# Optimization experiments

Hardware: AMD Instinct MI355X
Metric: run time of the kernel (lower is better)

## Reference

```python
import jax, jax.numpy as jnp
import numpy as np

T, B, H, E, V, L = 256, 32, 1024, 1024, 32000, 2


def lstm_stack(x, h0, c0, Wih, Whh, bih, bhh):
    # x: [T,B,E]; Wih/Whh: [L,4H,H]; bih/bhh: [L,4H]; h0/c0: [L,B,H]
    for l in range(Wih.shape[0]):
        Wi, Wh, bi, bh = Wih[l], Whh[l], bih[l], bhh[l]

        def step(carry, xt, Wi=Wi, Wh=Wh, bi=bi, bh=bh):
            h, c = carry
            g = xt @ Wi.T + h @ Wh.T + bi + bh  # [B,4H]
            i_, f_, g_, o_ = jnp.split(g, 4, axis=-1)  # PyTorch gate order i,f,g,o
            c = jax.nn.sigmoid(f_) * c + jax.nn.sigmoid(i_) * jnp.tanh(g_)
            h = jax.nn.sigmoid(o_) * jnp.tanh(c)
            return (h, c), h

        (_, _), x = jax.lax.scan(step, (h0[l], c0[l]), x)
    return x  # [T,B,H]


def setup_inputs() -> dict:
    key = jax.random.key(0)
    ks = jax.random.split(key, 20)
    u = lambda k, s: jax.random.uniform(k, s, jnp.float32, -0.1, 0.1)
    n = lambda k, s: 0.02 * jax.random.normal(k, s, jnp.float32)
    return {
        'data_left': jax.random.randint(ks[0], (T, B), 0, V),
        'data_right': jax.random.randint(ks[1], (T, B), 0, V),
        'h0_left': jnp.zeros((L, B, H), jnp.float32),
        'c0_left': jnp.zeros((L, B, H), jnp.float32),
        'h0_right': jnp.zeros((L, B, H), jnp.float32),
        'c0_right': jnp.zeros((L, B, H), jnp.float32),
        'emb': u(ks[2], (V, E)),
        'Wih_l': n(ks[3], (L, 4 * H, H)), 'Whh_l': n(ks[4], (L, 4 * H, H)),
        'bih_l': n(ks[5], (L, 4 * H)), 'bhh_l': n(ks[6], (L, 4 * H)),
        'Wih_r': n(ks[7], (L, 4 * H, H)), 'Whh_r': n(ks[8], (L, 4 * H, H)),
        'bih_r': n(ks[9], (L, 4 * H)), 'bhh_r': n(ks[10], (L, 4 * H)),
        'attn_w': n(ks[11], (1, 3 * H)), 'attn_b': n(ks[12], (1,)),
        'trans_w': n(ks[13], (H, 3 * H)), 'trans_b': n(ks[14], (H,)),
        'dec_w': u(ks[15], (V, H)), 'dec_b': jnp.zeros((V,), jnp.float32),
    }


def reference(data_left, data_right, h0_left, c0_left, h0_right, c0_right,
              emb, Wih_l, Whh_l, bih_l, bhh_l, Wih_r, Whh_r, bih_r, bhh_r,
              attn_w, attn_b, trans_w, trans_b, dec_w, dec_b):
    # Encode (dropout=0 -> identity). Right branch runs on the flipped sequence.
    xL = emb[data_left]                    # [T,B,E]
    xR = emb[data_right[::-1]]             # [T,B,E]
    outL = lstm_stack(xL, h0_left, c0_left, Wih_l, Whh_l, bih_l, bhh_l)   # [T,B,H]
    outR = lstm_stack(xR, h0_right, c0_right, Wih_r, Whh_r, bih_r, bhh_r)[::-1]

    # attn Linear(3H,1) splits into per-chunk projections: [left_i, right_i, ctx_k]
    w1, w2, w3 = jnp.split(attn_w[0], 3)   # each [H]
    a = outL @ w1 + outR @ w2 + attn_b[0]  # [T,B] query-dependent part
    sL = outL @ w3                          # [T,B]
    sR = outR @ w3                          # [T,B]

    # context for query i has fixed length T+1: k<=i -> outL[k], k>i -> outR[k-1]
    kk = jnp.arange(T + 1)
    ii = jnp.arange(T)
    maskL = kk[None, :] <= ii[:, None]      # [T,T+1]
    sL_pad = jnp.concatenate([sL, jnp.zeros((1, B), sL.dtype)], 0)   # [T+1,B]
    sR_sh = jnp.concatenate([jnp.zeros((1, B), sR.dtype), sR], 0)    # sR[k-1]
    ctx_s = jnp.where(maskL[:, :, None], sL_pad[None], sR_sh[None])  # [T,T+1,B]
    scores = jnp.tanh(a[:, None, :] + ctx_s)                          # [T,T+1,B]
    p = jax.nn.softmax(scores, axis=1)

    pL = p * maskL[:, :, None]
    pR = p * (~maskL)[:, :, None]
    # context_vector[i] = sum_k p[i,k] * ctx[i,k]
    cv = (jnp.einsum('ikb,kbh->ibh', pL[:, :T], outL)
          + jnp.einsum('ikb,kbh->ibh', pR[:, 1:], outR))              # [T,B,H]

    h3 = jnp.concatenate([outL, outR, cv], axis=-1)                   # [T,B,3H]
    pred = jnp.tanh(h3 @ trans_w.T + trans_b)                         # [T,B,H]
    decoded = pred @ dec_w.T + dec_b                                  # [T,B,V]
    return decoded
```

## Files before the change

### kernel.cpp

```cpp
#include <hip/hip_runtime.h>
#include <hip/hip_bf16.h>


using bf16 = __hip_bfloat16;
typedef __attribute__((ext_vector_type(8))) __bf16 bf16x8;
typedef __attribute__((ext_vector_type(4))) float f32x4;
typedef __attribute__((ext_vector_type(4))) short short4v;

#define T_ 256
#define B_ 32
#define H_ 1024
#define V_ 32000

__device__ __forceinline__ float b2f(bf16 x) { return __bfloat162float(x); }
__device__ __forceinline__ bf16 f2b(float x) { return __float2bfloat16(x); }
__device__ __forceinline__ float us2f(unsigned short u) {
  union { unsigned u; float f; } w; w.u = ((unsigned)u) << 16; return w.f;
}
__device__ __forceinline__ void st4(bf16* dst, float4 f) {
  union { bf16 h[4]; short4v s; } u;
  u.h[0] = f2b(f.x); u.h[1] = f2b(f.y); u.h[2] = f2b(f.z); u.h[3] = f2b(f.w);
  *reinterpret_cast<short4v*>(dst) = u.s;
}
__device__ __forceinline__ bf16x8 cvt8(float4 a, float4 b) {
  union { bf16 h[8]; bf16x8 v; } u;
  u.h[0] = f2b(a.x); u.h[1] = f2b(a.y); u.h[2] = f2b(a.z); u.h[3] = f2b(a.w);
  u.h[4] = f2b(b.x); u.h[5] = f2b(b.y); u.h[6] = f2b(b.z); u.h[7] = f2b(b.w);
  return u.v;
}

__global__ __launch_bounds__(256)
void cvt_f32_bf16(const float* __restrict__ src, bf16* __restrict__ dst, long n)
{
  long i = ((long)blockIdx.x * 256 + threadIdx.x) * 8;
  if (i >= n) return;
  float4 a = *reinterpret_cast<const float4*>(src + i);
  float4 b = *reinterpret_cast<const float4*>(src + i + 4);
  st4(dst + i, a); st4(dst + i + 4, b);
}

__global__ __launch_bounds__(128)
void embed_gather(const int* __restrict__ dl, const int* __restrict__ dr,
                  const float* __restrict__ emb,
                  bf16* __restrict__ xL, bf16* __restrict__ xR)
{
  int wg = blockIdx.x;
  int d  = wg >> 13;
  int r  = wg & 8191;
  int t  = r >> 5, b = r & 31;
  int tok = d ? dr[(T_ - 1 - t) * B_ + b] : dl[r];
  const float* src = emb + (long)tok * H_;
  bf16* dst = (d ? xR : xL) + (long)r * H_;
  int e = threadIdx.x * 8;
  float4 a = *reinterpret_cast<const float4*>(src + e);
  float4 c = *reinterpret_cast<const float4*>(src + e + 4);
  st4(dst + e, a); st4(dst + e + 4, c);
}

#define LSTRIDE 40

template<int ACT, int HASBIAS, int OUTF32>
__global__ __launch_bounds__(256)
void gemm_bt(const bf16* __restrict__ A, const float* __restrict__ Bwf,
             const float* __restrict__ bias, void* __restrict__ Cv,
             int M, int N, int K)
{
  __shared__ __align__(16) bf16 As[128 * LSTRIDE];
  __shared__ __align__(16) bf16 Bs[128 * LSTRIDE];
  const int tid  = threadIdx.x;
  const int lane = tid & 63;
  const int wave = tid >> 6;
  const int wm = wave >> 1, wn = wave & 1;
  const long bm = blockIdx.x, bn = blockIdx.y;

  const bf16*  Ag = A + bm * 128 * (long)K;
  const float* Bg = Bwf + bn * 128 * (long)K;

  f32x4 acc[4][4] = {};

  const int nk = K >> 5;
  for (int kt = 0; kt < nk; ++kt) {
    const int k0 = kt * 32;
    __syncthreads();
    #pragma unroll
    for (int j = 0; j < 2; ++j) {
      int chunk = j * 256 + tid;
      int row = chunk >> 2, c4 = chunk & 3;
      *reinterpret_cast<bf16x8*>(&As[row * LSTRIDE + c4 * 8]) =
          *reinterpret_cast<const bf16x8*>(&Ag[(long)row * K + k0 + c4 * 8]);
    }
    #pragma unroll
    for (int j = 0; j < 4; ++j) {
      int chunk = j * 256 + tid;
      int row = chunk >> 3, c4f = chunk & 7;
      float4 f = *reinterpret_cast<const float4*>(&Bg[(long)row * K + k0 + c4f * 4]);
      st4(&Bs[row * LSTRIDE + c4f * 4], f);
    }
    __syncthreads();
    bf16x8 af[4], bfr[4];
    #pragma unroll
    for (int m = 0; m < 4; ++m)
      af[m] = *reinterpret_cast<const bf16x8*>(
          &As[(wm * 64 + m * 16 + (lane & 15)) * LSTRIDE + (lane >> 4) * 8]);
    #pragma unroll
    for (int n = 0; n < 4; ++n)
      bfr[n] = *reinterpret_cast<const bf16x8*>(
          &Bs[(wn * 64 + n * 16 + (lane & 15)) * LSTRIDE + (lane >> 4) * 8]);
    #pragma unroll
    for (int m = 0; m < 4; ++m)
      #pragma unroll
      for (int n = 0; n < 4; ++n)
        acc[m][n] = __builtin_amdgcn_mfma_f32_16x16x32_bf16(af[m], bfr[n], acc[m][n], 0, 0, 0);
  }

  #pragma unroll
  for (int m = 0; m < 4; ++m) {
    int row = (int)bm * 128 + wm * 64 + m * 16 + ((lane >> 4) << 2);
    #pragma unroll
    for (int n = 0; n < 4; ++n) {
      int col = (int)bn * 128 + wn * 64 + n * 16 + (lane & 15);
      float bv = HASBIAS ? bias[col] : 0.f;
      #pragma unroll
      for (int j = 0; j < 4; ++j) {
        float v = acc[m][n][j] + bv;
        if (ACT) v = tanhf(v);
        long off = (long)(row + j) * N + col;
        if (OUTF32) reinterpret_cast<float*>(Cv)[off] = v;
        else        reinterpret_cast<bf16*>(Cv)[off] = f2b(v);
      }
    }
  }
}

__global__ __launch_bounds__(256, 1)
void lstm_layer(const bf16* __restrict__ WhhL, const bf16* __restrict__ WhhR,
                const bf16* __restrict__ giL,  const bf16* __restrict__ giR,
                const float* __restrict__ bihL, const float* __restrict__ bhhL,
                const float* __restrict__ bihR, const float* __restrict__ bhhR,
                const float* __restrict__ h0L, const float* __restrict__ h0R,
                const float* __restrict__ c0L, const float* __restrict__ c0R,
                bf16* __restrict__ houtL, bf16* __restrict__ houtR,
                int revR, unsigned* __restrict__ bar)
{
  const int d    = blockIdx.y;
  const int u0   = blockIdx.x * 16;
  const int tid  = threadIdx.x;
  const int lane = tid & 63;
  const int wq   = tid >> 6;
  const long BH  = (long)B_ * H_;

  const bf16*  Whh = d ? WhhR : WhhL;
  const bf16*  gi0 = d ? giR  : giL;
  const float* bi  = d ? bihR : bihL;
  const float* bh  = d ? bhhR : bhhL;
  const float* h0  = d ? h0R  : h0L;
  const float* c0  = d ? c0R  : c0L;
  bf16* hout       = d ? houtR : houtL;
  const int rev    = d ? revR : 0;
  unsigned* cnt    = bar + d;

  (void)__hip_atomic_load(cnt, __ATOMIC_ACQUIRE, __HIP_MEMORY_SCOPE_AGENT);

  const int klo = (lane >> 4) * 8;

  bf16x8 w_reg[4][8];
  #pragma unroll
  for (int g = 0; g < 4; ++g) {
    const bf16* p = Whh + ((long)g * H_ + u0 + (lane & 15)) * H_ + wq * 256 + klo;
    #pragma unroll
    for (int q = 0; q < 8; ++q)
      w_reg[g][q] = *reinterpret_cast<const bf16x8*>(p + q * 32);
  }

  const int b  = tid >> 3;
  const int u  = (tid & 7) * 2;
  const int ug = u0 + u;

  float bsum[4][2];
  #pragma unroll
  for (int g = 0; g < 4; ++g) {
    bsum[g][0] = bi[g * H_ + ug]     + bh[g * H_ + ug];
    bsum[g][1] = bi[g * H_ + ug + 1] + bh[g * H_ + ug + 1];
  }
  float cc0 = c0[(long)b * H_ + ug];
  float cc1 = c0[(long)b * H_ + ug + 1];

  __shared__ float gbuf[4][4][32][16];

  for (int s = 0; s < T_; ++s) {
    unsigned giv[4];
    {
      const bf16* gis = gi0 + (long)s * (B_ * 4 * H_) + (long)b * (4 * H_);
      #pragma unroll
      for (int g = 0; g < 4; ++g)
        giv[g] = *reinterpret_cast<const unsigned*>(&gis[g * H_ + ug]);
    }

    f32x4 acc[4][2];
    #pragma unroll
    for (int g = 0; g < 4; ++g) {
      acc[g][0] = f32x4{0.f, 0.f, 0.f, 0.f};
      acc[g][1] = f32x4{0.f, 0.f, 0.f, 0.f};
    }

    if (s == 0) {
      const float* ap0 = h0 + (long)(lane & 15) * H_ + wq * 256 + klo;
      const float* ap1 = ap0 + 16L * H_;
      #pragma unroll
      for (int q = 0; q < 8; ++q) {
        bf16x8 a0 = cvt8(*reinterpret_cast<const float4*>(ap0 + q * 32),
                         *reinterpret_cast<const float4*>(ap0 + q * 32 + 4));
        bf16x8 a1 = cvt8(*reinterpret_cast<const float4*>(ap1 + q * 32),
                         *reinterpret_cast<const float4*>(ap1 + q * 32 + 4));
        #pragma unroll
        for (int g = 0; g < 4; ++g) {
          acc[g][0] = __builtin_amdgcn_mfma_f32_16x16x32_bf16(a0, w_reg[g][q], acc[g][0], 0, 0, 0);
          acc[g][1] = __builtin_amdgcn_mfma_f32_16x16x32_bf16(a1, w_reg[g][q], acc[g][1], 0, 0, 0);
        }
      }
    } else {
      const bf16* hp  = hout + (long)(rev ? (T_ - s) : (s - 1)) * BH;
      const bf16* ap0 = hp + (long)(lane & 15) * H_ + wq * 256 + klo;
      const bf16* ap1 = ap0 + 16L * H_;
      #pragma unroll
      for (int q = 0; q < 8; ++q) {
        bf16x8 a0 = *reinterpret_cast<const bf16x8*>(ap0 + q * 32);
        bf16x8 a1 = *reinterpret_cast<const bf16x8*>(ap1 + q * 32);
        #pragma unroll
        for (int g = 0; g < 4; ++g) {
          acc[g][0] = __builtin_amdgcn_mfma_f32_16x16x32_bf16(a0, w_reg[g][q], acc[g][0], 0, 0, 0);
          acc[g][1] = __builtin_amdgcn_mfma_f32_16x16x32_bf16(a1, w_reg[g][q], acc[g][1], 0, 0, 0);
        }
      }
    }

    {
      int cr = (lane >> 4) << 2, ccu = lane & 15;
      #pragma unroll
      for (int g = 0; g < 4; ++g)
        #pragma unroll
        for (int j = 0; j < 4; ++j) {
          gbuf[wq][g][cr + j][ccu]      = acc[g][0][j];
          gbuf[wq][g][16 + cr + j][ccu] = acc[g][1][j];
        }
    }
    __syncthreads();

    {
      float g4[4][2];
      #pragma unroll
      for (int g = 0; g < 4; ++g) {
        float p0 = gbuf[0][g][b][u]     + gbuf[1][g][b][u];
        float p1 = gbuf[2][g][b][u]     + gbuf[3][g][b][u];
        float q0 = gbuf[0][g][b][u + 1] + gbuf[1][g][b][u + 1];
        float q1 = gbuf[2][g][b][u + 1] + gbuf[3][g][b][u + 1];
        g4[g][0] = (p0 + p1) + us2f((unsigned short)(giv[g] & 0xffffu)) + bsum[g][0];
        g4[g][1] = (q0 + q1) + us2f((unsigned short)(giv[g] >> 16))     + bsum[g][1];
      }
      float si0 = 1.f / (1.f + expf(-g4[0][0])), si1 = 1.f / (1.f + expf(-g4[0][1]));
      float sf0 = 1.f / (1.f + expf(-g4[1][0])), sf1 = 1.f / (1.f + expf(-g4[1][1]));
      float tg0 = tanhf(g4[2][0]),               tg1 = tanhf(g4[2][1]);
      float so0 = 1.f / (1.f + expf(-g4[3][0])), so1 = 1.f / (1.f + expf(-g4[3][1]));
      cc0 = sf0 * cc0 + si0 * tg0;
      cc1 = sf1 * cc1 + si1 * tg1;
      float hn0 = so0 * tanhf(cc0);
      float hn1 = so1 * tanhf(cc1);
      union { bf16 h[2]; unsigned w; } up;
      up.h[0] = f2b(hn0); up.h[1] = f2b(hn1);
      long wIdx = rev ? (long)(T_ - 1 - s) : (long)s;
      __hip_atomic_store(
          reinterpret_cast<unsigned*>(&hout[wIdx * BH + (long)b * H_ + ug]),
          up.w, __ATOMIC_RELAXED, __HIP_MEMORY_SCOPE_AGENT);
    }

    if (s + 1 < T_) {
      __syncthreads();
      if (tid == 0) {
        __hip_atomic_fetch_add(cnt, 1u, __ATOMIC_RELAXED, __HIP_MEMORY_SCOPE_AGENT);
        unsigned tgt = 64u * (unsigned)(s + 1);
        while (__hip_atomic_load(cnt, __ATOMIC_RELAXED, __HIP_MEMORY_SCOPE_AGENT) < tgt)
          __builtin_amdgcn_s_sleep(2);
      }
      __syncthreads();
    }
  }
}

__global__ __launch_bounds__(256)
void attn_scores(const bf16* __restrict__ outL, const bf16* __restrict__ outR,
                 const float* __restrict__ attn_w, const float* __restrict__ attn_b,
                 float* __restrict__ a, float* __restrict__ sL, float* __restrict__ sR)
{
  int r = blockIdx.x;
  int tid = threadIdx.x;
  const bf16* oL = outL + (long)r * H_;
  const bf16* oR = outR + (long)r * H_;
  int e = tid * 4;
  float pa = 0.f, pl = 0.f, pr = 0.f;
  #pragma unroll
  for (int j = 0; j < 4; ++j) {
    float l_ = b2f(oL[e + j]), r_ = b2f(oR[e + j]);
    float w1 = attn_w[e + j];
    float w2 = attn_w[H_ + e + j];
    float w3 = attn_w[2 * H_ + e + j];
    pa += w1 * l_ + w2 * r_;
    pl += w3 * l_;
    pr += w3 * r_;
  }
  #pragma unroll
  for (int off = 32; off > 0; off >>= 1) {
    pa += __shfl_down(pa, off);
    pl += __shfl_down(pl, off);
    pr += __shfl_down(pr, off);
  }
  __shared__ float red[3][4];
  int wave = tid >> 6, lane = tid & 63;
  if (lane == 0) { red[0][wave] = pa; red[1][wave] = pl; red[2][wave] = pr; }
  __syncthreads();
  if (tid == 0) {
    a[r]  = red[0][0] + red[0][1] + red[0][2] + red[0][3] + attn_b[0];
    sL[r] = red[1][0] + red[1][1] + red[1][2] + red[1][3];
    sR[r] = red[2][0] + red[2][1] + red[2][2] + red[2][3];
  }
}

__global__ __launch_bounds__(64)
void attn_softmax(const float* __restrict__ a, const float* __restrict__ sL,
                  const float* __restrict__ sR, float* __restrict__ p)
{
  int i = blockIdx.x, b = blockIdx.y;
  int lane = threadIdx.x;
  float av = a[i * B_ + b];
  float sc[5];
  float mx = -1e30f;
  #pragma unroll
  for (int q = 0; q < 5; ++q) {
    int k = lane + q * 64;
    float v = -1e30f;
    if (k < 257) {
      float ctx = (k <= i) ? sL[k * B_ + b] : sR[(k - 1) * B_ + b];
      v = tanhf(av + ctx);
    }
    sc[q] = v;
    mx = fmaxf(mx, v);
  }
  #pragma unroll
  for (int off = 32; off > 0; off >>= 1) mx = fmaxf(mx, __shfl_xor(mx, off));
  float sum = 0.f;
  #pragma unroll
  for (int q = 0; q < 5; ++q) {
    int k = lane + q * 64;
    float e = (k < 257) ? __expf(sc[q] - mx) : 0.f;
    sc[q] = e; sum += e;
  }
  #pragma unroll
  for (int off = 32; off > 0; off >>= 1) sum += __shfl_xor(sum, off);
  float inv = 1.f / sum;
  long base = ((long)b * T_ + i) * 257;
  #pragma unroll
  for (int q = 0; q < 5; ++q) {
    int k = lane + q * 64;
    if (k < 257) p[base + k] = sc[q] * inv;
  }
}

__global__ __launch_bounds__(256)
void h3_copy(const bf16* __restrict__ outL, const bf16* __restrict__ outR,
             bf16* __restrict__ h3)
{
  long gid = (long)blockIdx.x * 256 + threadIdx.x;
  long e = gid * 8;
  if (e >= (long)T_ * B_ * H_) return;
  long r = e >> 10; int h = (int)(e & 1023);
  *reinterpret_cast<bf16x8*>(&h3[r * 3 * H_ + h]) =
      *reinterpret_cast<const bf16x8*>(&outL[e]);
  *reinterpret_cast<bf16x8*>(&h3[r * 3 * H_ + H_ + h]) =
      *reinterpret_cast<const bf16x8*>(&outR[e]);
}

__global__ __launch_bounds__(256)
void attn_cv(const float* __restrict__ p, const bf16* __restrict__ outL,
             const bf16* __restrict__ outR, bf16* __restrict__ h3)
{
  int b = blockIdx.y;
  int i0 = blockIdx.x * 16;
  int tid = threadIdx.x;
  __shared__ float ps[16][257];
  for (int idx = tid; idx < 16 * 257; idx += 256) {
    int ii = idx / 257, k = idx % 257;
    ps[ii][k] = p[((long)b * T_ + i0 + ii) * 257 + k];
  }
  __syncthreads();
  float acc[16][4] = {};
  int h0 = tid * 4;
  for (int k = 0; k < 257; ++k) {
    float vL[4] = {0.f, 0.f, 0.f, 0.f}, vR[4] = {0.f, 0.f, 0.f, 0.f};
    if (k < 256) {
      short4v v = *reinterpret_cast<const short4v*>(&outL[((long)k * B_ + b) * H_ + h0]);
      vL[0] = us2f((unsigned short)v[0]); vL[1] = us2f((unsigned short)v[1]);
      vL[2] = us2f((unsigned short)v[2]); vL[3] = us2f((unsigned short)v[3]);
    }
    if (k >= 1) {
      short4v v = *reinterpret_cast<const short4v*>(&outR[((long)(k - 1) * B_ + b) * H_ + h0]);
      vR[0] = us2f((unsigned short)v[0]); vR[1] = us2f((unsigned short)v[1]);
      vR[2] = us2f((unsigned short)v[2]); vR[3] = us2f((unsigned short)v[3]);
    }
    #pragma unroll
    for (int ii = 0; ii < 16; ++ii) {
      float pv = ps[ii][k];
      bool useL = (i0 + ii) >= k;
      #pragma unroll
      for (int j = 0; j < 4; ++j)
        acc[ii][j] += pv * (useL ? vL[j] : vR[j]);
    }
  }
  #pragma unroll
  for (int ii = 0; ii < 16; ++ii)
    #pragma unroll
    for (int j = 0; j < 4; ++j)
      h3[((long)(i0 + ii) * B_ + b) * 3 * H_ + 2 * H_ + h0 + j] = f2b(acc[ii][j]);
}

extern "C" void kernel_launch(void* const* d_in, const int* in_sizes, int n_in,
                              void* d_out, int out_size, void* d_ws, size_t ws_size,
                              hipStream_t stream)
{
  (void)in_sizes; (void)n_in; (void)out_size; (void)ws_size;
  const int*   data_left  = (const int*)  d_in[0];
  const int*   data_right = (const int*)  d_in[1];
  const float* h0_left    = (const float*)d_in[2];
  const float* c0_left    = (const float*)d_in[3];
  const float* h0_right   = (const float*)d_in[4];
  const float* c0_right   = (const float*)d_in[5];
  const float* emb        = (const float*)d_in[6];
  const float* Wih_l      = (const float*)d_in[7];
  const float* Whh_l      = (const float*)d_in[8];
  const float* bih_l      = (const float*)d_in[9];
  const float* bhh_l      = (const float*)d_in[10];
  const float* Wih_r      = (const float*)d_in[11];
  const float* Whh_r      = (const float*)d_in[12];
  const float* bih_r      = (const float*)d_in[13];
  const float* bhh_r      = (const float*)d_in[14];
  const float* attn_w     = (const float*)d_in[15];
  const float* attn_b     = (const float*)d_in[16];
  const float* trans_w    = (const float*)d_in[17];
  const float* trans_b    = (const float*)d_in[18];
  const float* dec_w      = (const float*)d_in[19];
  const float* dec_b      = (const float*)d_in[20];

  char* ws = (char*)d_ws;
  bf16*     XL   = (bf16*)    (ws + 0L);
  bf16*     XR   = (bf16*)    (ws + 16777216L);
  bf16*     GI_L = (bf16*)    (ws + 33554432L);
  bf16*     GI_R = (bf16*)    (ws + 100663296L);
  bf16*     H0L  = (bf16*)    (ws + 167772160L);
  bf16*     H0R  = (bf16*)    (ws + 184549376L);
  unsigned* BAR  = (unsigned*)(ws + 201326592L);
  bf16*     WHHB = (bf16*)    (ws + 201588736L);
  bf16*  O1L  = XL;
  bf16*  O1R  = XR;
  bf16*  H3   = GI_L;
  float* P_   = (float*)(ws + 100663296L);
  float* A_   = (float*)(ws + 109084672L);
  float* SL_  = (float*)(ws + 109117440L);
  float* SR_  = (float*)(ws + 109150208L);
  bf16*  PRED = (bf16*) (ws + 109182976L);

  const long BH  = (long)B_ * H_;
  const long WL  = 4L * H_ * H_;
  bf16* WHHB_l = WHHB;
  bf16* WHHB_r = WHHB + 2 * WL;

  cvt_f32_bf16<<<4096, 256, 0, stream>>>(Whh_l, WHHB_l, 2 * WL);
  cvt_f32_bf16<<<4096, 256, 0, stream>>>(Whh_r, WHHB_r, 2 * WL);

  embed_gather<<<16384, 128, 0, stream>>>(data_left, data_right, emb, XL, XR);

  gemm_bt<0,0,0><<<dim3(64, 32), 256, 0, stream>>>(XL, Wih_l, nullptr, GI_L, 8192, 4096, 1024);
  gemm_bt<0,0,0><<<dim3(64, 32), 256, 0, stream>>>(XR, Wih_r, nullptr, GI_R, 8192, 4096, 1024);

  hipMemsetAsync(BAR, 0, 64, stream);
  lstm_layer<<<dim3(64, 2), 256, 0, stream>>>(
      WHHB_l, WHHB_r, GI_L, GI_R,
      bih_l, bhh_l, bih_r, bhh_r,
      h0_left, h0_right, c0_left, c0_right,
      H0L, H0R, 0, BAR);

  gemm_bt<0,0,0><<<dim3(64, 32), 256, 0, stream>>>(H0L, Wih_l + WL, nullptr, GI_L, 8192, 4096, 1024);
  gemm_bt<0,0,0><<<dim3(64, 32), 256, 0, stream>>>(H0R, Wih_r + WL, nullptr, GI_R, 8192, 4096, 1024);

  hipMemsetAsync(BAR, 0, 64, stream);
  lstm_layer<<<dim3(64, 2), 256, 0, stream>>>(
      WHHB_l + WL, WHHB_r + WL, GI_L, GI_R,
      bih_l + 4 * H_, bhh_l + 4 * H_, bih_r + 4 * H_, bhh_r + 4 * H_,
      h0_left + BH, h0_right + BH, c0_left + BH, c0_right + BH,
      O1L, O1R, 1, BAR);

  attn_scores<<<8192, 256, 0, stream>>>(O1L, O1R, attn_w, attn_b, A_, SL_, SR_);
  attn_softmax<<<dim3(256, 32), 64, 0, stream>>>(A_, SL_, SR_, P_);
  h3_copy<<<4096, 256, 0, stream>>>(O1L, O1R, H3);
  attn_cv<<<dim3(16, 32), 256, 0, stream>>>(P_, O1L, O1R, H3);

  gemm_bt<1,1,0><<<dim3(64, 8),   256, 0, stream>>>(H3,   trans_w, trans_b, PRED, 8192, 1024, 3072);
  gemm_bt<0,1,1><<<dim3(64, 250), 256, 0, stream>>>(PRED, dec_w,   dec_b,   d_out, 8192, 32000, 1024);
}
```

Measured before the change: 4.784 ms.

## Fuse both LSTM layers into one wavefront-pipelined persistent kernel

Replaces the two sequential lstm_layer launches and the layer-1 input-projection GEMMs with a single persistent kernel of 384 blocks, split into three roles: layer-0 recurrence, a per-timestep layer-1 input projection that writes into a 4-slot ring buffer, and layer-1 recurrence. The roles synchronise through global atomic counters and per-block flags. Layer 1 can then run one step behind layer 0 instead of waiting for the whole of layer 0, which hides most of one full recurrent pass. In exchange, the layer-1 input projection becomes a small per-step MFMA job rather than a large efficient GEMM. Correctness depends on all 384 blocks being co-resident (two per CU under the launch bounds), and the extra spin-wait synchronisation adds per-step latency.

```diff
diff --git a/kernel.cpp b/kernel.cpp
--- a/kernel.cpp
+++ b/kernel.cpp
@@ -27,6 +27,10 @@
   u.h[0] = f2b(a.x); u.h[1] = f2b(a.y); u.h[2] = f2b(a.z); u.h[3] = f2b(a.w);
   u.h[4] = f2b(b.x); u.h[5] = f2b(b.y); u.h[6] = f2b(b.z); u.h[7] = f2b(b.w);
   return u.v;
+}
+__device__ __forceinline__ void poll_ge(unsigned* p, unsigned tgt) {
+  while (__hip_atomic_load(p, __ATOMIC_RELAXED, __HIP_MEMORY_SCOPE_AGENT) < tgt)
+    __builtin_amdgcn_s_sleep(2);
 }
 
 __global__ __launch_bounds__(256)
@@ -132,36 +136,149 @@
   }
 }
 
-__global__ __launch_bounds__(256, 1)
-void lstm_layer(const bf16* __restrict__ WhhL, const bf16* __restrict__ WhhR,
-                const bf16* __restrict__ giL,  const bf16* __restrict__ giR,
-                const float* __restrict__ bihL, const float* __restrict__ bhhL,
-                const float* __restrict__ bihR, const float* __restrict__ bhhR,
-                const float* __restrict__ h0L, const float* __restrict__ h0R,
-                const float* __restrict__ c0L, const float* __restrict__ c0R,
-                bf16* __restrict__ houtL, bf16* __restrict__ houtR,
-                int revR, unsigned* __restrict__ bar)
-{
-  const int d    = blockIdx.y;
-  const int u0   = blockIdx.x * 16;
+__device__ __forceinline__ void mfma_h_bf16(const bf16* hp, int lane, int wq, int klo,
+                                            const bf16x8 w[4][8], f32x4 acc[4][2])
+{
+  const bf16* ap0 = hp + (long)(lane & 15) * H_ + wq * 256 + klo;
+  const bf16* ap1 = ap0 + 16L * H_;
+  #pragma unroll
+  for (int q = 0; q < 8; ++q) {
+    bf16x8 a0 = *reinterpret_cast<const bf16x8*>(ap0 + q * 32);
+    bf16x8 a1 = *reinterpret_cast<const bf16x8*>(ap1 + q * 32);
+    #pragma unroll
+    for (int g = 0; g < 4; ++g) {
+      acc[g][0] = __builtin_amdgcn_mfma_f32_16x16x32_bf16(a0, w[g][q], acc[g][0], 0, 0, 0);
+      acc[g][1] = __builtin_amdgcn_mfma_f32_16x16x32_bf16(a1, w[g][q], acc[g][1], 0, 0, 0);
+    }
+  }
+}
+__device__ __forceinline__ void mfma_h_f32(const float* hp, int lane, int wq, int klo,
+                                           const bf16x8 w[4][8], f32x4 acc[4][2])
+{
+  const float* ap0 = hp + (long)(lane & 15) * H_ + wq * 256 + klo;
+  const float* ap1 = ap0 + 16L * H_;
+  #pragma unroll
+  for (int q = 0; q < 8; ++q) {
+    bf16x8 a0 = cvt8(*reinterpret_cast<const float4*>(ap0 + q * 32),
+                     *reinterpret_cast<const float4*>(ap0 + q * 32 + 4));
+    bf16x8 a1 = cvt8(*reinterpret_cast<const float4*>(ap1 + q * 32),
+                     *reinterpret_cast<const float4*>(ap1 + q * 32 + 4));
+    #pragma unroll
+    for (int g = 0; g < 4; ++g) {
+      acc[g][0] = __builtin_amdgcn_mfma_f32_16x16x32_bf16(a0, w[g][q], acc[g][0], 0, 0, 0);
+      acc[g][1] = __builtin_amdgcn_mfma_f32_16x16x32_bf16(a1, w[g][q], acc[g][1], 0, 0, 0);
+    }
+  }
+}
+
+__global__ __launch_bounds__(256, 2)
+void lstm_fused(const bf16* __restrict__ Whh0L, const bf16* __restrict__ Whh0R,
+                const bf16* __restrict__ Whh1L, const bf16* __restrict__ Whh1R,
+                const float* __restrict__ Wih1Lf, const float* __restrict__ Wih1Rf,
+                const bf16* __restrict__ gi0L, const bf16* __restrict__ gi0R,
+                bf16* __restrict__ gi1ring,
+                const float* __restrict__ bih_l, const float* __restrict__ bhh_l,
+                const float* __restrict__ bih_r, const float* __restrict__ bhh_r,
+                const float* __restrict__ h0_left, const float* __restrict__ h0_right,
+                const float* __restrict__ c0_left, const float* __restrict__ c0_right,
+                bf16* __restrict__ H0L, bf16* __restrict__ H0R,
+                bf16* __restrict__ O1L, bf16* __restrict__ O1R,
+                unsigned* __restrict__ bar)
+{
   const int tid  = threadIdx.x;
   const int lane = tid & 63;
   const int wq   = tid >> 6;
   const long BH  = (long)B_ * H_;
-
-  const bf16*  Whh = d ? WhhR : WhhL;
-  const bf16*  gi0 = d ? giR  : giL;
-  const float* bi  = d ? bihR : bihL;
-  const float* bh  = d ? bhhR : bhhL;
-  const float* h0  = d ? h0R  : h0L;
-  const float* c0  = d ? c0R  : c0L;
-  bf16* hout       = d ? houtR : houtL;
-  const int rev    = d ? revR : 0;
-  unsigned* cnt    = bar + d;
-
-  (void)__hip_atomic_load(cnt, __ATOMIC_ACQUIRE, __HIP_MEMORY_SCOPE_AGENT);
-
+  const long B4H = (long)B_ * 4 * H_;
+  const int grp  = blockIdx.x >> 6;
+  const int rank = blockIdx.x & 63;
+  const int role = grp >> 1;
+  const int d    = grp & 1;
+
+  (void)__hip_atomic_load(bar + 8, __ATOMIC_ACQUIRE, __HIP_MEMORY_SCOPE_AGENT);
+
+  unsigned* cntL0 = bar + d;
+  unsigned* cntL1 = bar + 2 + d;
+  unsigned* flg   = bar + 16 + d * 64;
+
+  const int u0  = rank * 16;
   const int klo = (lane >> 4) * 8;
+  const int b   = tid >> 3;
+  const int u   = (tid & 7) * 2;
+  const int ug  = u0 + u;
+
+  __shared__ float gbuf[4][4][32][16];
+
+  if (role == 1) {
+    const float* wf  = d ? Wih1Rf : Wih1Lf;
+    const bf16*  h0s = d ? H0R : H0L;
+    bf16* ring = gi1ring + (long)d * 4 * B4H;
+
+    bf16x8 w_reg[4][8];
+    #pragma unroll
+    for (int g = 0; g < 4; ++g) {
+      const float* p = wf + ((long)g * H_ + u0 + (lane & 15)) * H_ + wq * 256 + klo;
+      #pragma unroll
+      for (int q = 0; q < 8; ++q)
+        w_reg[g][q] = cvt8(*reinterpret_cast<const float4*>(p + q * 32),
+                           *reinterpret_cast<const float4*>(p + q * 32 + 4));
+    }
+
+    for (int t = 0; t < T_; ++t) {
+      if (tid == 0) {
+        poll_ge(cntL0, 64u * (unsigned)(t + 1));
+        if (t >= 4) poll_ge(cntL1, 64u * (unsigned)(t - 3));
+      }
+      __syncthreads();
+
+      f32x4 acc[4][2] = {};
+      mfma_h_bf16(h0s + (long)t * BH, lane, wq, klo, w_reg, acc);
+
+      {
+        int cr = (lane >> 4) << 2, ccu = lane & 15;
+        #pragma unroll
+        for (int g = 0; g < 4; ++g)
+          #pragma unroll
+          for (int j = 0; j < 4; ++j) {
+            gbuf[wq][g][cr + j][ccu]      = acc[g][0][j];
+            gbuf[wq][g][16 + cr + j][ccu] = acc[g][1][j];
+          }
+      }
+      __syncthreads();
+
+      {
+        bf16* slot = ring + (long)(t & 3) * B4H + (long)b * (4 * H_);
+        #pragma unroll
+        for (int g = 0; g < 4; ++g) {
+          float v0 = (gbuf[0][g][b][u]     + gbuf[1][g][b][u])
+                   + (gbuf[2][g][b][u]     + gbuf[3][g][b][u]);
+          float v1 = (gbuf[0][g][b][u + 1] + gbuf[1][g][b][u + 1])
+                   + (gbuf[2][g][b][u + 1] + gbuf[3][g][b][u + 1]);
+          union { bf16 h[2]; unsigned w; } pk;
+          pk.h[0] = f2b(v0); pk.h[1] = f2b(v1);
+          __hip_atomic_store(reinterpret_cast<unsigned*>(&slot[g * H_ + ug]),
+                             pk.w, __ATOMIC_RELAXED, __HIP_MEMORY_SCOPE_AGENT);
+        }
+      }
+      __syncthreads();
+      if (tid == 0)
+        __hip_atomic_store(flg + rank, (unsigned)(t + 1),
+                           __ATOMIC_RELAXED, __HIP_MEMORY_SCOPE_AGENT);
+    }
+    return;
+  }
+
+  const int isL1 = (role == 2);
+  const bf16*  Whh = isL1 ? (d ? Whh1R : Whh1L) : (d ? Whh0R : Whh0L);
+  const bf16*  gi0 = d ? gi0R : gi0L;
+  const bf16*  ring = gi1ring + (long)d * 4 * B4H;
+  const float* bi  = (d ? bih_r : bih_l) + (isL1 ? 4 * H_ : 0);
+  const float* bh  = (d ? bhh_r : bhh_l) + (isL1 ? 4 * H_ : 0);
+  const float* h0i = (d ? h0_right : h0_left) + (isL1 ? BH : 0);
+  const float* c0i = (d ? c0_right : c0_left) + (isL1 ? BH : 0);
+  bf16* hout = isL1 ? (d ? O1R : O1L) : (d ? H0R : H0L);
+  const int rev = (isL1 && d) ? 1 : 0;
+  unsigned* cnt = isL1 ? cntL1 : cntL0;
 
   bf16x8 w_reg[4][8];
   #pragma unroll
@@ -171,10 +288,6 @@
     for (int q = 0; q < 8; ++q)
       w_reg[g][q] = *reinterpret_cast<const bf16x8*>(p + q * 32);
   }
-
-  const int b  = tid >> 3;
-  const int u  = (tid & 7) * 2;
-  const int ug = u0 + u;
 
   float bsum[4][2];
   #pragma unroll
@@ -182,56 +295,38 @@
     bsum[g][0] = bi[g * H_ + ug]     + bh[g * H_ + ug];
     bsum[g][1] = bi[g * H_ + ug + 1] + bh[g * H_ + ug + 1];
   }
-  float cc0 = c0[(long)b * H_ + ug];
-  float cc1 = c0[(long)b * H_ + ug + 1];
-
-  __shared__ float gbuf[4][4][32][16];
+  float cc0 = c0i[(long)b * H_ + ug];
+  float cc1 = c0i[(long)b * H_ + ug + 1];
 
   for (int s = 0; s < T_; ++s) {
+    if (isL1) {
+      if (tid == 0) {
+        poll_ge(flg + rank, (unsigned)(s + 1));
+        if (s >= 1) poll_ge(cnt, 64u * (unsigned)s);
+      }
+      __syncthreads();
+    }
+
     unsigned giv[4];
-    {
-      const bf16* gis = gi0 + (long)s * (B_ * 4 * H_) + (long)b * (4 * H_);
+    if (isL1) {
+      const bf16* gis = ring + (long)(s & 3) * B4H + (long)b * (4 * H_);
+      #pragma unroll
+      for (int g = 0; g < 4; ++g)
+        giv[g] = __hip_atomic_load(
+            reinterpret_cast<const unsigned*>(&gis[g * H_ + ug]),
+            __ATOMIC_RELAXED, __HIP_MEMORY_SCOPE_AGENT);
+    } else {
+      const bf16* gis = gi0 + (long)s * B4H + (long)b * (4 * H_);
       #pragma unroll
       for (int g = 0; g < 4; ++g)
         giv[g] = *reinterpret_cast<const unsigned*>(&gis[g * H_ + ug]);
     }
 
-    f32x4 acc[4][2];
-    #pragma unroll
-    for (int g = 0; g < 4; ++g) {
-      acc[g][0] = f32x4{0.f, 0.f, 0.f, 0.f};
-      acc[g][1] = f32x4{0.f, 0.f, 0.f, 0.f};
-    }
-
+    f32x4 acc[4][2] = {};
     if (s == 0) {
-      const float* ap0 = h0 + (long)(lane & 15) * H_ + wq * 256 + klo;
-      const float* ap1 = ap0 + 16L * H_;
-      #pragma unroll
-      for (int q = 0; q < 8; ++q) {
-        bf16x8 a0 = cvt8(*reinterpret_cast<const float4*>(ap0 + q * 32),
-                         *reinterpret_cast<const float4*>(ap0 + q * 32 + 4));
-        bf16x8 a1 = cvt8(*reinterpret_cast<const float4*>(ap1 + q * 32),
-                         *reinterpret_cast<const float4*>(ap1 + q * 32 + 4));
-        #pragma unroll
-        for (int g = 0; g < 4; ++g) {
-          acc[g][0] = __builtin_amdgcn_mfma_f32_16x16x32_bf16(a0, w_reg[g][q], acc[g][0], 0, 0, 0);
-          acc[g][1] = __builtin_amdgcn_mfma_f32_16x16x32_bf16(a1, w_reg[g][q], acc[g][1], 0, 0, 0);
-        }
-      }
+      mfma_h_f32(h0i, lane, wq, klo, w_reg, acc);
     } else {
-      const bf16* hp  = hout + (long)(rev ? (T_ - s) : (s - 1)) * BH;
-      const bf16* ap0 = hp + (long)(lane & 15) * H_ + wq * 256 + klo;
-      const bf16* ap1 = ap0 + 16L * H_;
-      #pragma unroll
-      for (int q = 0; q < 8; ++q) {
-        bf16x8 a0 = *reinterpret_cast<const bf16x8*>(ap0 + q * 32);
-        bf16x8 a1 = *reinterpret_cast<const bf16x8*>(ap1 + q * 32);
-        #pragma unroll
-        for (int g = 0; g < 4; ++g) {
-          acc[g][0] = __builtin_amdgcn_mfma_f32_16x16x32_bf16(a0, w_reg[g][q], acc[g][0], 0, 0, 0);
-          acc[g][1] = __builtin_amdgcn_mfma_f32_16x16x32_bf16(a1, w_reg[g][q], acc[g][1], 0, 0, 0);
-        }
-      }
+      mfma_h_bf16(hout + (long)(rev ? (T_ - s) : (s - 1)) * BH, lane, wq, klo, w_reg, acc);
     }
 
     {
@@ -273,16 +368,13 @@
           up.w, __ATOMIC_RELAXED, __HIP_MEMORY_SCOPE_AGENT);
     }
 
-    if (s + 1 < T_) {
-      __syncthreads();
-      if (tid == 0) {
-        __hip_atomic_fetch_add(cnt, 1u, __ATOMIC_RELAXED, __HIP_MEMORY_SCOPE_AGENT);
-        unsigned tgt = 64u * (unsigned)(s + 1);
-        while (__hip_atomic_load(cnt, __ATOMIC_RELAXED, __HIP_MEMORY_SCOPE_AGENT) < tgt)
-          __builtin_amdgcn_s_sleep(2);
-      }
-      __syncthreads();
-    }
+    __syncthreads();
+    if (tid == 0) {
+      __hip_atomic_fetch_add(cnt, 1u, __ATOMIC_RELAXED, __HIP_MEMORY_SCOPE_AGENT);
+      if (!isL1 && s + 1 < T_)
+        poll_ge(cnt, 64u * (unsigned)(s + 1));
+    }
+    __syncthreads();
   }
 }
 
@@ -457,6 +549,7 @@
   bf16*     H0R  = (bf16*)    (ws + 184549376L);
   unsigned* BAR  = (unsigned*)(ws + 201326592L);
   bf16*     WHHB = (bf16*)    (ws + 201588736L);
+  bf16*     GI1  = (bf16*)    (ws + 235143168L);
   bf16*  O1L  = XL;
   bf16*  O1R  = XR;
   bf16*  H3   = GI_L;
@@ -466,7 +559,6 @@
   float* SR_  = (float*)(ws + 109150208L);
   bf16*  PRED = (bf16*) (ws + 109182976L);
 
-  const long BH  = (long)B_ * H_;
   const long WL  = 4L * H_ * H_;
   bf16* WHHB_l = WHHB;
   bf16* WHHB_r = WHHB + 2 * WL;
@@ -479,22 +571,14 @@
   gemm_bt<0,0,0><<<dim3(64, 32), 256, 0, stream>>>(XL, Wih_l, nullptr, GI_L, 8192, 4096, 1024);
   gemm_bt<0,0,0><<<dim3(64, 32), 256, 0, stream>>>(XR, Wih_r, nullptr, GI_R, 8192, 4096, 1024);
 
-  hipMemsetAsync(BAR, 0, 64, stream);
-  lstm_layer<<<dim3(64, 2), 256, 0, stream>>>(
-      WHHB_l, WHHB_r, GI_L, GI_R,
+  hipMemsetAsync(BAR, 0, 2048, stream);
+  lstm_fused<<<384, 256, 0, stream>>>(
+      WHHB_l, WHHB_r, WHHB_l + WL, WHHB_r + WL,
+      Wih_l + WL, Wih_r + WL,
+      GI_L, GI_R, GI1,
       bih_l, bhh_l, bih_r, bhh_r,
       h0_left, h0_right, c0_left, c0_right,
-      H0L, H0R, 0, BAR);
-
-  gemm_bt<0,0,0><<<dim3(64, 32), 256, 0, stream>>>(H0L, Wih_l + WL, nullptr, GI_L, 8192, 4096, 1024);
-  gemm_bt<0,0,0><<<dim3(64, 32), 256, 0, stream>>>(H0R, Wih_r + WL, nullptr, GI_R, 8192, 4096, 1024);
-
-  hipMemsetAsync(BAR, 0, 64, stream);
-  lstm_layer<<<dim3(64, 2), 256, 0, stream>>>(
-      WHHB_l + WL, WHHB_r + WL, GI_L, GI_R,
-      bih_l + 4 * H_, bhh_l + 4 * H_, bih_r + 4 * H_, bhh_r + 4 * H_,
-      h0_left + BH, h0_right + BH, c0_left + BH, c0_right + BH,
-      O1L, O1R, 1, BAR);
+      H0L, H0R, O1L, O1R, BAR);
 
   attn_scores<<<8192, 256, 0, stream>>>(O1L, O1R, attn_w, attn_b, A_, SL_, SR_);
   attn_softmax<<<dim3(256, 32), 64, 0, stream>>>(A_, SL_, SR_, P_);
```

After: 6.477 ms. 1.35x slower.

## Pre-convert GEMM weights to bf16 and load tiles via direct global-to-LDS

Applied to the files above, without the earlier changes.

Adds a gemm_bb kernel whose A and B operands are both bf16. Tiles are loaded with global_load_lds straight into a swizzled LDS layout instead of going through registers with an fp32-to-bf16 conversion. Wih, trans_w and dec_w are converted to bf16 up front, when the workspace is large enough, so the big GEMMs read half the weight bytes and skip per-tile conversion. This costs extra conversion launches and workspace memory, and the old path stays as a fallback when the workspace is too small.

```diff
diff --git a/kernel.cpp b/kernel.cpp
--- a/kernel.cpp
+++ b/kernel.cpp
@@ -27,6 +27,11 @@
   u.h[0] = f2b(a.x); u.h[1] = f2b(a.y); u.h[2] = f2b(a.z); u.h[3] = f2b(a.w);
   u.h[4] = f2b(b.x); u.h[5] = f2b(b.y); u.h[6] = f2b(b.z); u.h[7] = f2b(b.w);
   return u.v;
+}
+__device__ __forceinline__ void gload_lds16(const bf16* g, bf16* l) {
+  __builtin_amdgcn_global_load_lds(
+      (const __attribute__((address_space(1))) void*)g,
+      (__attribute__((address_space(3))) void*)l, 16, 0, 0);
 }
 
 __global__ __launch_bounds__(256)
@@ -106,6 +111,74 @@
     for (int n = 0; n < 4; ++n)
       bfr[n] = *reinterpret_cast<const bf16x8*>(
           &Bs[(wn * 64 + n * 16 + (lane & 15)) * LSTRIDE + (lane >> 4) * 8]);
+    #pragma unroll
+    for (int m = 0; m < 4; ++m)
+      #pragma unroll
+      for (int n = 0; n < 4; ++n)
+        acc[m][n] = __builtin_amdgcn_mfma_f32_16x16x32_bf16(af[m], bfr[n], acc[m][n], 0, 0, 0);
+  }
+
+  #pragma unroll
+  for (int m = 0; m < 4; ++m) {
+    int row = (int)bm * 128 + wm * 64 + m * 16 + ((lane >> 4) << 2);
+    #pragma unroll
+    for (int n = 0; n < 4; ++n) {
+      int col = (int)bn * 128 + wn * 64 + n * 16 + (lane & 15);
+      float bv = HASBIAS ? bias[col] : 0.f;
+      #pragma unroll
+      for (int j = 0; j < 4; ++j) {
+        float v = acc[m][n][j] + bv;
+        if (ACT) v = tanhf(v);
+        long off = (long)(row + j) * N + col;
+        if (OUTF32) reinterpret_cast<float*>(Cv)[off] = v;
+        else        reinterpret_cast<bf16*>(Cv)[off] = f2b(v);
+      }
+    }
+  }
+}
+
+template<int ACT, int HASBIAS, int OUTF32>
+__global__ __launch_bounds__(256)
+void gemm_bb(const bf16* __restrict__ A, const bf16* __restrict__ Bw,
+             const float* __restrict__ bias, void* __restrict__ Cv,
+             int M, int N, int K)
+{
+  __shared__ __align__(16) bf16 As[128 * 32];
+  __shared__ __align__(16) bf16 Bs[128 * 32];
+  const int tid  = threadIdx.x;
+  const int lane = tid & 63;
+  const int wave = tid >> 6;
+  const int wm = wave >> 1, wn = wave & 1;
+  const long bm = blockIdx.x, bn = blockIdx.y;
+
+  const bf16* Ag = A  + bm * 128 * (long)K;
+  const bf16* Bg = Bw + bn * 128 * (long)K;
+
+  const int r0  = tid >> 2;
+  const int cgd = (tid & 3) ^ (r0 & 3);
+  const int rsw = ((lane >> 4) ^ (lane & 3)) * 8;
+
+  f32x4 acc[4][4] = {};
+  const int nk = K >> 5;
+  for (int kt = 0; kt < nk; ++kt) {
+    const int k0 = kt * 32;
+    __syncthreads();
+    #pragma unroll
+    for (int j = 0; j < 2; ++j) {
+      int row = j * 64 + r0;
+      gload_lds16(Ag + (long)row * K + k0 + cgd * 8, As + (j * 256 + wave * 64) * 8);
+      gload_lds16(Bg + (long)row * K + k0 + cgd * 8, Bs + (j * 256 + wave * 64) * 8);
+    }
+    __syncthreads();
+    bf16x8 af[4], bfr[4];
+    #pragma unroll
+    for (int m = 0; m < 4; ++m)
+      af[m] = *reinterpret_cast<const bf16x8*>(
+          &As[(wm * 64 + m * 16 + (lane & 15)) * 32 + rsw]);
+    #pragma unroll
+    for (int n = 0; n < 4; ++n)
+      bfr[n] = *reinterpret_cast<const bf16x8*>(
+          &Bs[(wn * 64 + n * 16 + (lane & 15)) * 32 + rsw]);
     #pragma unroll
     for (int m = 0; m < 4; ++m)
       #pragma unroll
@@ -425,7 +498,7 @@
                               void* d_out, int out_size, void* d_ws, size_t ws_size,
                               hipStream_t stream)
 {
-  (void)in_sizes; (void)n_in; (void)out_size; (void)ws_size;
+  (void)in_sizes; (void)n_in; (void)out_size;
   const int*   data_left  = (const int*)  d_in[0];
   const int*   data_right = (const int*)  d_in[1];
   const float* h0_left    = (const float*)d_in[2];
@@ -457,6 +530,10 @@
   bf16*     H0R  = (bf16*)    (ws + 184549376L);
   unsigned* BAR  = (unsigned*)(ws + 201326592L);
   bf16*     WHHB = (bf16*)    (ws + 201588736L);
+  bf16*     WIHB   = (bf16*)  (ws + 235143168L);
+  bf16*     TRANSB = (bf16*)  (ws + 268697600L);
+  bf16*     DECB   = (bf16*)  (ws + 274989056L);
+  const bool fast = ws_size >= 340525056UL;
   bf16*  O1L  = XL;
   bf16*  O1R  = XR;
   bf16*  H3   = GI_L;
@@ -470,26 +547,44 @@
   const long WL  = 4L * H_ * H_;
   bf16* WHHB_l = WHHB;
   bf16* WHHB_r = WHHB + 2 * WL;
+  bf16* WIHB_l = WIHB;
+  bf16* WIHB_r = WIHB + 2 * WL;
 
   cvt_f32_bf16<<<4096, 256, 0, stream>>>(Whh_l, WHHB_l, 2 * WL);
   cvt_f32_bf16<<<4096, 256, 0, stream>>>(Whh_r, WHHB_r, 2 * WL);
+  if (fast) {
+    cvt_f32_bf16<<<4096, 256, 0, stream>>>(Wih_l, WIHB_l, 2 * WL);
+    cvt_f32_bf16<<<4096, 256, 0, stream>>>(Wih_r, WIHB_r, 2 * WL);
+    cvt_f32_bf16<<<1536, 256, 0, stream>>>(trans_w, TRANSB, (long)H_ * 3 * H_);
+    cvt_f32_bf16<<<16000, 256, 0, stream>>>(dec_w, DECB, (long)V_ * H_);
+  }
 
   embed_gather<<<16384, 128, 0, stream>>>(data_left, data_right, emb, XL, XR);
 
-  gemm_bt<0,0,0><<<dim3(64, 32), 256, 0, stream>>>(XL, Wih_l, nullptr, GI_L, 8192, 4096, 1024);
-  gemm_bt<0,0,0><<<dim3(64, 32), 256, 0, stream>>>(XR, Wih_r, nullptr, GI_R, 8192, 4096, 1024);
-
-  hipMemsetAsync(BAR, 0, 64, stream);
+  if (fast) {
+    gemm_bb<0,0,0><<<dim3(64, 32), 256, 0, stream>>>(XL, WIHB_l, nullptr, GI_L, 8192, 4096, 1024);
+    gemm_bb<0,0,0><<<dim3(64, 32), 256, 0, stream>>>(XR, WIHB_r, nullptr, GI_R, 8192, 4096, 1024);
+  } else {
+    gemm_bt<0,0,0><<<dim3(64, 32), 256, 0, stream>>>(XL, Wih_l, nullptr, GI_L, 8192, 4096, 1024);
+    gemm_bt<0,0,0><<<dim3(64, 32), 256, 0, stream>>>(XR, Wih_r, nullptr, GI_R, 8192, 4096, 1024);
+  }
+
+  hipMemsetAsync(BAR, 0, 256, stream);
   lstm_layer<<<dim3(64, 2), 256, 0, stream>>>(
       WHHB_l, WHHB_r, GI_L, GI_R,
       bih_l, bhh_l, bih_r, bhh_r,
       h0_left, h0_right, c0_left, c0_right,
       H0L, H0R, 0, BAR);
 
-  gemm_bt<0,0,0><<<dim3(64, 32), 256, 0, stream>>>(H0L, Wih_l + WL, nullptr, GI_L, 8192, 4096, 1024);
-  gemm_bt<0,0,0><<<dim3(64, 32), 256, 0, stream>>>(H0R, Wih_r + WL, nullptr, GI_R, 8192, 4096, 1024);
-
-  hipMemsetAsync(BAR, 0, 64, stream);
+  if (fast) {
+    gemm_bb<0,0,0><<<dim3(64, 32), 256, 0, stream>>>(H0L, WIHB_l + WL, nullptr, GI_L, 8192, 4096, 1024);
+    gemm_bb<0,0,0><<<dim3(64, 32), 256, 0, stream>>>(H0R, WIHB_r + WL, nullptr, GI_R, 8192, 4096, 1024);
+  } else {
+    gemm_bt<0,0,0><<<dim3(64, 32), 256, 0, stream>>>(H0L, Wih_l + WL, nullptr, GI_L, 8192, 4096, 1024);
+    gemm_bt<0,0,0><<<dim3(64, 32), 256, 0, stream>>>(H0R, Wih_r + WL, nullptr, GI_R, 8192, 4096, 1024);
+  }
+
+  hipMemsetAsync(BAR, 0, 256, stream);
   lstm_layer<<<dim3(64, 2), 256, 0, stream>>>(
       WHHB_l + WL, WHHB_r + WL, GI_L, GI_R,
       bih_l + 4 * H_, bhh_l + 4 * H_, bih_r + 4 * H_, bhh_r + 4 * H_,
@@ -501,6 +596,11 @@
   h3_copy<<<4096, 256, 0, stream>>>(O1L, O1R, H3);
   attn_cv<<<dim3(16, 32), 256, 0, stream>>>(P_, O1L, O1R, H3);
 
-  gemm_bt<1,1,0><<<dim3(64, 8),   256, 0, stream>>>(H3,   trans_w, trans_b, PRED, 8192, 1024, 3072);
-  gemm_bt<0,1,1><<<dim3(64, 250), 256, 0, stream>>>(PRED, dec_w,   dec_b,   d_out, 8192, 32000, 1024);
-}
+  if (fast) {
+    gemm_bb<1,1,0><<<dim3(64, 8),   256, 0, stream>>>(H3,   TRANSB, trans_b, PRED, 8192, 1024, 3072);
+    gemm_bb<0,1,1><<<dim3(64, 250), 256, 0, stream>>>(PRED, DECB,   dec_b,   d_out, 8192, 32000, 1024);
+  } else {
+    gemm_bt<1,1,0><<<dim3(64, 8),   256, 0, stream>>>(H3,   trans_w, trans_b, PRED, 8192, 1024, 3072);
+    gemm_bt<0,1,1><<<dim3(64, 250), 256, 0, stream>>>(PRED, dec_w,   dec_b,   d_out, 8192, 32000, 1024);
+  }
+}
```

New measurement: 4.461 ms. 6.8% less time.
